# Optimization experiments

Measured on AMD Instinct MI355X. Metric: run time of the kernel, lower is better.

## Reference

```python
import jax, jax.numpy as jnp
import numpy as np

B, D, E, K = 8192, 1024, 8, 5  # batch, in_dim, num_size_classes, num_depth_classes
H = max(64, D)                 # hidden = max(64, in_dim)
EPS = 1e-8


def ordinal_logits_to_probs(logits, num_classes):
    # logits: [B, K-1] cumulative ordinal logits -> [B, K] class probs
    q = jax.nn.sigmoid(logits)
    probs = jnp.concatenate(
        [1.0 - q[:, :1], q[:, :-1] - q[:, 1:], q[:, -1:]], axis=1
    )  # [B, K]
    probs = jnp.clip(probs, EPS)
    return probs / jnp.clip(probs.sum(axis=1, keepdims=True), EPS)


def setup_inputs() -> dict:
    key = jax.random.key(0)
    kx, ks, k1, k2 = jax.random.split(key, 4)
    x = jax.random.normal(kx, (B, D), dtype=jnp.float32)
    size_idx = jax.random.randint(ks, (B,), 0, E, dtype=jnp.int64)
    # per-expert 2-layer MLP params: Linear(D,H) -> ReLU -> Linear(H,K-1)
    W1 = jax.random.normal(k1, (E, D, H), dtype=jnp.float32) / np.sqrt(D)
    b1 = jnp.zeros((E, H), dtype=jnp.float32)
    W2 = jax.random.normal(k2, (E, H, K - 1), dtype=jnp.float32) / np.sqrt(H)
    b2 = jnp.zeros((E, K - 1), dtype=jnp.float32)
    return {"x": x, "size_idx": size_idx, "W1": W1, "b1": b1, "W2": W2, "b2": b2}


def reference(x, size_idx, W1, b1, W2, b2):
    # Hard routing: each token gets the output of expert size_idx[b].
    # Dense all-expert compute + per-token select (same math as mask/gather/scatter,
    # dropout is inference-mode identity).
    h = jax.nn.relu(jnp.einsum('bd,edh->beh', x, W1) + b1)      # [B, E, H]
    all_logits = jnp.einsum('beh,ehk->bek', h, W2) + b2          # [B, E, K-1]
    idx = size_idx.astype(jnp.int32)[:, None, None]              # [B, 1, 1]
    logits = jnp.take_along_axis(all_logits, idx, axis=1)[:, 0]  # [B, K-1]
    probs = ordinal_logits_to_probs(logits, K)                   # [B, K]
    return logits, probs
```

## Files before the change

kernel.cpp:

```cpp
#include <hip/hip_runtime.h>
#include <cstdint>
#include <cstddef>

#define Bn 8192
#define Dn 1024
#define Hn 1024
#define En 8
#define MT 128
#define NB 16
#define MTILES (Bn / MT + En)
#define PERM_N (Bn + En * MT)

typedef unsigned short u16;
typedef __bf16 bf16x8 __attribute__((ext_vector_type(8)));
typedef float f32x4 __attribute__((ext_vector_type(4)));
typedef unsigned short ushort8 __attribute__((ext_vector_type(8)));

__device__ __forceinline__ u16 f2bf(float f) {
  unsigned int u = __float_as_uint(f);
  unsigned int r = u + 0x7fffu + ((u >> 16) & 1u);
  return (u16)(r >> 16);
}

__device__ __forceinline__ void gld16(const void* g, void* l) {
  __builtin_amdgcn_global_load_lds(
      (const __attribute__((address_space(1))) void*)g,
      (__attribute__((address_space(3))) void*)l, 16, 0, 0);
}

#define PIPE_BARRIER_VM4() do {                    \
    asm volatile("" ::: "memory");                 \
    __builtin_amdgcn_s_waitcnt(0x0F74);            \
    __builtin_amdgcn_s_barrier();                  \
    asm volatile("" ::: "memory");                 \
  } while (0)
#define PIPE_BARRIER_VM0() do {                    \
    asm volatile("" ::: "memory");                 \
    __builtin_amdgcn_s_waitcnt(0x0F70);            \
    __builtin_amdgcn_s_barrier();                  \
    asm volatile("" ::: "memory");                 \
  } while (0)

__global__ __launch_bounds__(1024) void route_k(const int* __restrict__ sidx,
                                                int* __restrict__ off,
                                                int* __restrict__ perm) {
  __shared__ int hist[16][En];
  __shared__ int base[16][En];
  __shared__ int eoff[En + 1];
  int t = threadIdx.x;
  int wv = t >> 6;
  if (t < 16 * En) ((int*)hist)[t] = 0;
#pragma unroll
  for (int i = 0; i < PERM_N / 1024; i++) perm[t + i * 1024] = -1;
  __syncthreads();
  int e8[8], r8[8];
#pragma unroll
  for (int i = 0; i < 8; i++) {
    int e = sidx[t + i * 1024];
    e8[i] = e;
    r8[i] = atomicAdd(&hist[wv][e], 1);
  }
  __syncthreads();
  if (t < En) {
    int s = 0;
    for (int w = 0; w < 16; w++) { base[w][t] = s; s += hist[w][t]; }
    hist[0][t] = s;
  }
  __syncthreads();
  if (t == 0) {
    int o = 0;
    for (int e = 0; e < En; e++) {
      eoff[e] = o; off[e] = o;
      o += (hist[0][e] + MT - 1) & ~(MT - 1);
    }
    eoff[En] = o; off[En] = o;
  }
  __syncthreads();
#pragma unroll
  for (int i = 0; i < 8; i++) {
    int e = e8[i];
    perm[eoff[e] + base[wv][e] + r8[i]] = t + i * 1024;
  }
}

__global__ __launch_bounds__(256) void cvt_xp_k(const float* __restrict__ x,
                                                const int* __restrict__ perm,
                                                u16* __restrict__ xbp) {
  size_t idx = ((size_t)blockIdx.x * 256 + threadIdx.x) * 8;
  int p = (int)(idx >> 10);
  int col = (int)(idx & 1023);
  int tok = perm[p];
  ushort8 o;
  if (tok < 0) {
    o = (ushort8){0, 0, 0, 0, 0, 0, 0, 0};
  } else {
    const float* src = x + ((size_t)tok << 10) + col;
    float4 a = *(const float4*)src;
    float4 b = *(const float4*)(src + 4);
    o[0] = f2bf(a.x); o[1] = f2bf(a.y); o[2] = f2bf(a.z); o[3] = f2bf(a.w);
    o[4] = f2bf(b.x); o[5] = f2bf(b.y); o[6] = f2bf(b.z); o[7] = f2bf(b.w);
  }
  *(ushort8*)(xbp + idx) = o;
}

__global__ __launch_bounds__(256) void cvt_w1_k(const float* __restrict__ W1,
                                                u16* __restrict__ W1t) {
  __shared__ float tile[64][65];
  int e = blockIdx.z;
  int k0 = blockIdx.y * 64;
  int n0 = blockIdx.x * 64;
  int c4 = (threadIdx.x & 15) * 4;
  int r0 = threadIdx.x >> 4;
  const float* src = W1 + ((size_t)e << 20) + (size_t)k0 * Hn + n0;
#pragma unroll
  for (int i = 0; i < 4; i++) {
    int r = r0 + i * 16;
    float4 v = *(const float4*)(src + (size_t)r * Hn + c4);
    tile[r][c4 + 0] = v.x; tile[r][c4 + 1] = v.y;
    tile[r][c4 + 2] = v.z; tile[r][c4 + 3] = v.w;
  }
  __syncthreads();
  u16* dst = W1t + ((size_t)e << 20) + (size_t)n0 * Dn + k0;
#pragma unroll
  for (int i = 0; i < 4; i++) {
    int h = r0 + i * 16;
    ushort4 o;
    o.x = f2bf(tile[c4 + 0][h]);
    o.y = f2bf(tile[c4 + 1][h]);
    o.z = f2bf(tile[c4 + 2][h]);
    o.w = f2bf(tile[c4 + 3][h]);
    *(ushort4*)(dst + (size_t)h * Dn + c4) = o;
  }
}

__global__ __launch_bounds__(256) void gemm_k(
    const u16* __restrict__ xbp, const u16* __restrict__ w1t,
    const float* __restrict__ b1, const float* __restrict__ w2,
    const int* __restrict__ off, float* __restrict__ partials) {
  __shared__ u16 As[3][4096];
  __shared__ u16 Bs[3][4096];

  int n0 = blockIdx.x * 128;
  int row0 = blockIdx.y * MT;
  if (row0 >= off[En]) return;
  int e = 0;
  while (row0 >= off[e + 1]) e++;

  int tid = threadIdx.x;
  int lane = tid & 63, w = tid >> 6;
  int wm = w >> 1, wn = w & 1;

  int srow = lane >> 2;
  int slot = lane & 3;
  int scol = (slot ^ ((srow >> 1) & 3)) * 8;
  const u16* aG[2]; const u16* bG[2];
  int lOff[2];
#pragma unroll
  for (int j = 0; j < 2; j++) {
    int rl = 32 * w + 16 * j + srow;
    aG[j] = xbp + (size_t)(row0 + rl) * Dn + scol;
    bG[j] = w1t + ((size_t)e << 20) + (size_t)(n0 + rl) * Dn + scol;
    lOff[j] = (32 * w + 16 * j) * 32;
  }

  f32x4 acc[4][4];
#pragma unroll
  for (int i = 0; i < 4; i++)
#pragma unroll
    for (int j = 0; j < 4; j++)
      acc[i][j] = (f32x4){0.f, 0.f, 0.f, 0.f};

  int fr = lane & 15;
  int qf = lane >> 4;
  int qs = (qf ^ ((fr >> 1) & 3)) * 8;
  int offA[4], offB[4];
#pragma unroll
  for (int i = 0; i < 4; i++)
    offA[i] = (wm * 64 + i * 16 + fr) * 32 + qs;
#pragma unroll
  for (int j = 0; j < 4; j++)
    offB[j] = (wn * 64 + j * 16 + fr) * 32 + qs;

#pragma unroll
  for (int it = 0; it < 2; it++) {
    int ko = it * 32;
    gld16(aG[0] + ko, (u16*)As[it] + lOff[0]);
    gld16(aG[1] + ko, (u16*)As[it] + lOff[1]);
    gld16(bG[0] + ko, (u16*)Bs[it] + lOff[0]);
    gld16(bG[1] + ko, (u16*)Bs[it] + lOff[1]);
  }

#pragma unroll
  for (int i = 0; i < 31; i++) {
    PIPE_BARRIER_VM4();
    if (i + 2 < 32) {
      int s = (i + 2) % 3;
      int ko = (i + 2) * 32;
      gld16(aG[0] + ko, (u16*)As[s] + lOff[0]);
      gld16(aG[1] + ko, (u16*)As[s] + lOff[1]);
      gld16(bG[0] + ko, (u16*)Bs[s] + lOff[0]);
      gld16(bG[1] + ko, (u16*)Bs[s] + lOff[1]);
    }
    const u16* Ab = (const u16*)As[i % 3];
    const u16* Bb = (const u16*)Bs[i % 3];
    bf16x8 af[4], bfr[4];
#pragma unroll
    for (int ii = 0; ii < 4; ii++) af[ii] = *(const bf16x8*)(Ab + offA[ii]);
#pragma unroll
    for (int jj = 0; jj < 4; jj++) bfr[jj] = *(const bf16x8*)(Bb + offB[jj]);
#pragma unroll
    for (int ii = 0; ii < 4; ii++)
#pragma unroll
      for (int jj = 0; jj < 4; jj++)
        acc[ii][jj] = __builtin_amdgcn_mfma_f32_16x16x32_bf16(af[ii], bfr[jj], acc[ii][jj], 0, 0, 0);
  }
  {
    PIPE_BARRIER_VM0();
    const u16* Ab = (const u16*)As[31 % 3];
    const u16* Bb = (const u16*)Bs[31 % 3];
    bf16x8 af[4], bfr[4];
#pragma unroll
    for (int ii = 0; ii < 4; ii++) af[ii] = *(const bf16x8*)(Ab + offA[ii]);
#pragma unroll
    for (int jj = 0; jj < 4; jj++) bfr[jj] = *(const bf16x8*)(Bb + offB[jj]);
#pragma unroll
    for (int ii = 0; ii < 4; ii++)
#pragma unroll
      for (int jj = 0; jj < 4; jj++)
        acc[ii][jj] = __builtin_amdgcn_mfma_f32_16x16x32_bf16(af[ii], bfr[jj], acc[ii][jj], 0, 0, 0);
  }

  int fq = lane >> 4;
  float4 w2v[4]; float b1v[4];
#pragma unroll
  for (int j = 0; j < 4; j++) {
    int col = n0 + wn * 64 + j * 16 + fr;
    w2v[j] = *(const float4*)(w2 + ((size_t)e * Hn + col) * 4);
    b1v[j] = b1[(size_t)e * Hn + col];
  }
  int chunk = blockIdx.x * 2 + wn;
#pragma unroll
  for (int i = 0; i < 4; i++) {
    int rbase = wm * 64 + i * 16 + fq * 4;
#pragma unroll
    for (int r = 0; r < 4; r++) {
      float s0 = 0.f, s1 = 0.f, s2 = 0.f, s3 = 0.f;
#pragma unroll
      for (int j = 0; j < 4; j++) {
        float h = acc[i][j][r] + b1v[j];
        h = fmaxf(h, 0.f);
        s0 = fmaf(h, w2v[j].x, s0);
        s1 = fmaf(h, w2v[j].y, s1);
        s2 = fmaf(h, w2v[j].z, s2);
        s3 = fmaf(h, w2v[j].w, s3);
      }
#pragma unroll
      for (int m = 1; m < 16; m <<= 1) {
        s0 += __shfl_xor(s0, m);
        s1 += __shfl_xor(s1, m);
        s2 += __shfl_xor(s2, m);
        s3 += __shfl_xor(s3, m);
      }
      if (fr == 0) {
        int row = row0 + rbase + r;
        *(float4*)(partials + ((size_t)row * NB + chunk) * 4) =
            make_float4(s0, s1, s2, s3);
      }
    }
  }
}

__global__ void probs_k(const float* __restrict__ partials,
                        const int* __restrict__ perm, const int* __restrict__ off,
                        const int* __restrict__ sidx, const float* __restrict__ b2,
                        float* __restrict__ out) {
  int p = blockIdx.x * blockDim.x + threadIdx.x;
  if (p >= off[En]) return;
  int tok = perm[p];
  if (tok < 0) return;
  int e = sidx[tok];
  float s0 = 0.f, s1 = 0.f, s2 = 0.f, s3 = 0.f;
#pragma unroll
  for (int nb = 0; nb < NB; nb++) {
    float4 v = *(const float4*)(partials + ((size_t)p * NB + nb) * 4);
    s0 += v.x; s1 += v.y; s2 += v.z; s3 += v.w;
  }
  float l0 = s0 + b2[e * 4 + 0];
  float l1 = s1 + b2[e * 4 + 1];
  float l2 = s2 + b2[e * 4 + 2];
  float l3 = s3 + b2[e * 4 + 3];
  out[tok * 4 + 0] = l0; out[tok * 4 + 1] = l1;
  out[tok * 4 + 2] = l2; out[tok * 4 + 3] = l3;
  float q0 = 1.f / (1.f + expf(-l0));
  float q1 = 1.f / (1.f + expf(-l1));
  float q2 = 1.f / (1.f + expf(-l2));
  float q3 = 1.f / (1.f + expf(-l3));
  const float eps = 1e-8f;
  float p0 = fmaxf(1.f - q0, eps);
  float p1 = fmaxf(q0 - q1, eps);
  float p2 = fmaxf(q1 - q2, eps);
  float p3 = fmaxf(q2 - q3, eps);
  float p4 = fmaxf(q3, eps);
  float s = p0 + p1 + p2 + p3 + p4;
  float inv = 1.f / fmaxf(s, eps);
  float* pr = out + (size_t)Bn * 4 + (size_t)tok * 5;
  pr[0] = p0 * inv; pr[1] = p1 * inv; pr[2] = p2 * inv;
  pr[3] = p3 * inv; pr[4] = p4 * inv;
}

extern "C" void kernel_launch(void* const* d_in, const int* in_sizes, int n_in,
                              void* d_out, int out_size, void* d_ws, size_t ws_size,
                              hipStream_t stream) {
  const float* x  = (const float*)d_in[0];
  const int* sidx = (const int*)d_in[1];
  const float* W1 = (const float*)d_in[2];
  const float* b1 = (const float*)d_in[3];
  const float* W2 = (const float*)d_in[4];
  const float* b2 = (const float*)d_in[5];
  float* out = (float*)d_out;

  uint8_t* w = (uint8_t*)d_ws;
  int* off  = (int*)(w + 64);
  int* perm = (int*)(w + 512);
  u16* xbp      = (u16*)(w + 40960);
  u16* w1t      = (u16*)(w + 18919424);
  float* parts  = (float*)(w + 35700736);

  route_k<<<1, 1024, 0, stream>>>(sidx, off, perm);
  cvt_xp_k<<<(PERM_N * Dn) / (256 * 8), 256, 0, stream>>>(x, perm, xbp);
  cvt_w1_k<<<dim3(Hn / 64, Dn / 64, En), 256, 0, stream>>>(W1, w1t);
  gemm_k<<<dim3(Hn / 128, MTILES), 256, 0, stream>>>(xbp, w1t, b1, W2, off, parts);
  probs_k<<<(PERM_N + 255) / 256, 256, 0, stream>>>(parts, perm, off, sidx, b2, out);
}
```

Before: 160.6 us.

## Parallelize routing, fuse W1 conversion with histogram, deepen GEMM pipeline to 4 stages

Replaces the single-block route kernel with a multi-block histogram, fused into the W1 transpose/convert kernel, followed by a multi-block ranking kernel that uses global atomics. The gather kernel now handles one row per block. The GEMM's LDS ring grows from 3 to 4 stages with a prefetch distance of 3, which adds shared memory and deeper in-flight loads. A memset and an extra launch are added, and token order within an expert becomes nondeterministic.

```diff
diff --git a/kernel.cpp b/kernel.cpp
--- a/kernel.cpp
+++ b/kernel.cpp
@@ -7,9 +7,9 @@
 #define Hn 1024
 #define En 8
 #define MT 128
+#define MTILES (PERM_N / MT)
+#define PERM_N (Bn + En * MT)
 #define NB 16
-#define MTILES (Bn / MT + En)
-#define PERM_N (Bn + En * MT)
 
 typedef unsigned short u16;
 typedef __bf16 bf16x8 __attribute__((ext_vector_type(8)));
@@ -28,108 +28,133 @@
       (__attribute__((address_space(3))) void*)l, 16, 0, 0);
 }
 
-#define PIPE_BARRIER_VM4() do {                    \
+#define PIPE_WAIT_BARRIER(imm) do {                \
     asm volatile("" ::: "memory");                 \
-    __builtin_amdgcn_s_waitcnt(0x0F74);            \
+    __builtin_amdgcn_s_waitcnt(imm);               \
     __builtin_amdgcn_s_barrier();                  \
     asm volatile("" ::: "memory");                 \
   } while (0)
-#define PIPE_BARRIER_VM0() do {                    \
-    asm volatile("" ::: "memory");                 \
-    __builtin_amdgcn_s_waitcnt(0x0F70);            \
-    __builtin_amdgcn_s_barrier();                  \
-    asm volatile("" ::: "memory");                 \
-  } while (0)
-
-__global__ __launch_bounds__(1024) void route_k(const int* __restrict__ sidx,
-                                                int* __restrict__ off,
-                                                int* __restrict__ perm) {
-  __shared__ int hist[16][En];
-  __shared__ int base[16][En];
-  __shared__ int eoff[En + 1];
+
+__global__ __launch_bounds__(256) void prep_k(const int* __restrict__ sidx,
+                                              const float* __restrict__ W1,
+                                              u16* __restrict__ w1t,
+                                              int* __restrict__ cnt) {
+  int bid = blockIdx.x;
   int t = threadIdx.x;
-  int wv = t >> 6;
-  if (t < 16 * En) ((int*)hist)[t] = 0;
-#pragma unroll
-  for (int i = 0; i < PERM_N / 1024; i++) perm[t + i * 1024] = -1;
-  __syncthreads();
-  int e8[8], r8[8];
-#pragma unroll
-  for (int i = 0; i < 8; i++) {
-    int e = sidx[t + i * 1024];
-    e8[i] = e;
-    r8[i] = atomicAdd(&hist[wv][e], 1);
-  }
-  __syncthreads();
-  if (t < En) {
-    int s = 0;
-    for (int w = 0; w < 16; w++) { base[w][t] = s; s += hist[w][t]; }
-    hist[0][t] = s;
-  }
-  __syncthreads();
-  if (t == 0) {
-    int o = 0;
-    for (int e = 0; e < En; e++) {
-      eoff[e] = o; off[e] = o;
-      o += (hist[0][e] + MT - 1) & ~(MT - 1);
-    }
-    eoff[En] = o; off[En] = o;
-  }
-  __syncthreads();
-#pragma unroll
-  for (int i = 0; i < 8; i++) {
-    int e = e8[i];
-    perm[eoff[e] + base[wv][e] + r8[i]] = t + i * 1024;
-  }
-}
-
-__global__ __launch_bounds__(256) void cvt_xp_k(const float* __restrict__ x,
+  if (bid < 8) {
+    __shared__ int hist[4][En];
+    int wv = t >> 6;
+    if (t < 4 * En) ((int*)hist)[t] = 0;
+    __syncthreads();
+#pragma unroll
+    for (int i = 0; i < 4; i++) {
+      int e = sidx[bid * 1024 + t + i * 256];
+      atomicAdd(&hist[wv][e], 1);
+    }
+    __syncthreads();
+    if (t < En) {
+      int s = hist[0][t] + hist[1][t] + hist[2][t] + hist[3][t];
+      atomicAdd(&cnt[t], s);
+    }
+  } else {
+    __shared__ float tile[64][65];
+    int wb = bid - 8;
+    int e = wb >> 8;
+    int k0 = ((wb >> 4) & 15) * 64;
+    int n0 = (wb & 15) * 64;
+    int c4 = (t & 15) * 4;
+    int r0 = t >> 4;
+    const float* src = W1 + ((size_t)e << 20) + (size_t)k0 * Hn + n0;
+#pragma unroll
+    for (int i = 0; i < 4; i++) {
+      int r = r0 + i * 16;
+      float4 v = *(const float4*)(src + (size_t)r * Hn + c4);
+      tile[r][c4 + 0] = v.x; tile[r][c4 + 1] = v.y;
+      tile[r][c4 + 2] = v.z; tile[r][c4 + 3] = v.w;
+    }
+    __syncthreads();
+    u16* dst = w1t + ((size_t)e << 20) + (size_t)n0 * Dn + k0;
+#pragma unroll
+    for (int i = 0; i < 4; i++) {
+      int h = r0 + i * 16;
+      ushort4 o;
+      o.x = f2bf(tile[c4 + 0][h]);
+      o.y = f2bf(tile[c4 + 1][h]);
+      o.z = f2bf(tile[c4 + 2][h]);
+      o.w = f2bf(tile[c4 + 3][h]);
+      *(ushort4*)(dst + (size_t)h * Dn + c4) = o;
+    }
+  }
+}
+
+__global__ __launch_bounds__(256) void rank_k(const int* __restrict__ sidx,
+                                              const int* __restrict__ cnt,
+                                              int* __restrict__ gcur,
+                                              int* __restrict__ off,
+                                              int* __restrict__ perm) {
+  int b = blockIdx.x, t = threadIdx.x;
+  int offl[En + 1];
+  int o = 0;
+#pragma unroll
+  for (int e = 0; e < En; e++) { offl[e] = o; o += (cnt[e] + MT - 1) & ~(MT - 1); }
+  offl[En] = o;
+
+  if (b < 32) {
+    __shared__ int hist[4][En];
+    __shared__ int wbase[4][En];
+    __shared__ int bbase[En];
+    int wv = t >> 6;
+    if (t < 4 * En) ((int*)hist)[t] = 0;
+    __syncthreads();
+    int tok = b * 256 + t;
+    int e = sidx[tok];
+    int r = atomicAdd(&hist[wv][e], 1);
+    __syncthreads();
+    if (t < En) {
+      int s = 0;
+#pragma unroll
+      for (int w = 0; w < 4; w++) { wbase[w][t] = s; s += hist[w][t]; }
+      bbase[t] = atomicAdd(&gcur[t], s);
+    }
+    __syncthreads();
+    int eo = offl[0];
+    int sel = e;
+    eo = (sel == 0) ? offl[0] : (sel == 1) ? offl[1] : (sel == 2) ? offl[2] :
+         (sel == 3) ? offl[3] : (sel == 4) ? offl[4] : (sel == 5) ? offl[5] :
+         (sel == 6) ? offl[6] : offl[7];
+    int dest = eo + bbase[e] + wbase[wv][e] + r;
+    perm[dest] = tok;
+  } else {
+    int e = b - 32;
+    int start = 0, end = 0, o2 = 0;
+#pragma unroll
+    for (int i = 0; i < En; i++) {
+      int pad = (cnt[i] + MT - 1) & ~(MT - 1);
+      if (i == e) { start = o2 + cnt[i]; end = o2 + pad; }
+      o2 += pad;
+    }
+    for (int p = start + t; p < end; p += 256) perm[p] = -1;
+    if (e == 0 && t == 0) {
+#pragma unroll
+      for (int i = 0; i <= En; i++) off[i] = offl[i];
+    }
+  }
+}
+
+__global__ __launch_bounds__(256) void gather_k(const float* __restrict__ x,
                                                 const int* __restrict__ perm,
                                                 u16* __restrict__ xbp) {
-  size_t idx = ((size_t)blockIdx.x * 256 + threadIdx.x) * 8;
-  int p = (int)(idx >> 10);
-  int col = (int)(idx & 1023);
+  int p = blockIdx.x;
+  int t = threadIdx.x;
   int tok = perm[p];
-  ushort8 o;
+  u16* dst = xbp + ((size_t)p << 10) + t * 4;
   if (tok < 0) {
-    o = (ushort8){0, 0, 0, 0, 0, 0, 0, 0};
+    *(ushort4*)dst = (ushort4){0, 0, 0, 0};
   } else {
-    const float* src = x + ((size_t)tok << 10) + col;
-    float4 a = *(const float4*)src;
-    float4 b = *(const float4*)(src + 4);
-    o[0] = f2bf(a.x); o[1] = f2bf(a.y); o[2] = f2bf(a.z); o[3] = f2bf(a.w);
-    o[4] = f2bf(b.x); o[5] = f2bf(b.y); o[6] = f2bf(b.z); o[7] = f2bf(b.w);
-  }
-  *(ushort8*)(xbp + idx) = o;
-}
-
-__global__ __launch_bounds__(256) void cvt_w1_k(const float* __restrict__ W1,
-                                                u16* __restrict__ W1t) {
-  __shared__ float tile[64][65];
-  int e = blockIdx.z;
-  int k0 = blockIdx.y * 64;
-  int n0 = blockIdx.x * 64;
-  int c4 = (threadIdx.x & 15) * 4;
-  int r0 = threadIdx.x >> 4;
-  const float* src = W1 + ((size_t)e << 20) + (size_t)k0 * Hn + n0;
-#pragma unroll
-  for (int i = 0; i < 4; i++) {
-    int r = r0 + i * 16;
-    float4 v = *(const float4*)(src + (size_t)r * Hn + c4);
-    tile[r][c4 + 0] = v.x; tile[r][c4 + 1] = v.y;
-    tile[r][c4 + 2] = v.z; tile[r][c4 + 3] = v.w;
-  }
-  __syncthreads();
-  u16* dst = W1t + ((size_t)e << 20) + (size_t)n0 * Dn + k0;
-#pragma unroll
-  for (int i = 0; i < 4; i++) {
-    int h = r0 + i * 16;
+    float4 v = *(const float4*)(x + ((size_t)tok << 10) + t * 4);
     ushort4 o;
-    o.x = f2bf(tile[c4 + 0][h]);
-    o.y = f2bf(tile[c4 + 1][h]);
-    o.z = f2bf(tile[c4 + 2][h]);
-    o.w = f2bf(tile[c4 + 3][h]);
-    *(ushort4*)(dst + (size_t)h * Dn + c4) = o;
+    o.x = f2bf(v.x); o.y = f2bf(v.y); o.z = f2bf(v.z); o.w = f2bf(v.w);
+    *(ushort4*)dst = o;
   }
 }
 
@@ -137,8 +162,8 @@
     const u16* __restrict__ xbp, const u16* __restrict__ w1t,
     const float* __restrict__ b1, const float* __restrict__ w2,
     const int* __restrict__ off, float* __restrict__ partials) {
-  __shared__ u16 As[3][4096];
-  __shared__ u16 Bs[3][4096];
+  __shared__ u16 As[4][4096];
+  __shared__ u16 Bs[4][4096];
 
   int n0 = blockIdx.x * 128;
   int row0 = blockIdx.y * MT;
@@ -182,7 +207,7 @@
     offB[j] = (wn * 64 + j * 16 + fr) * 32 + qs;
 
 #pragma unroll
-  for (int it = 0; it < 2; it++) {
+  for (int it = 0; it < 3; it++) {
     int ko = it * 32;
     gld16(aG[0] + ko, (u16*)As[it] + lOff[0]);
     gld16(aG[1] + ko, (u16*)As[it] + lOff[1]);
@@ -191,18 +216,20 @@
   }
 
 #pragma unroll
-  for (int i = 0; i < 31; i++) {
-    PIPE_BARRIER_VM4();
-    if (i + 2 < 32) {
-      int s = (i + 2) % 3;
-      int ko = (i + 2) * 32;
+  for (int i = 0; i < 32; i++) {
+    if (i <= 29)      PIPE_WAIT_BARRIER(0x0F78);
+    else if (i == 30) PIPE_WAIT_BARRIER(0x0F74);
+    else              PIPE_WAIT_BARRIER(0x0F70);
+    if (i + 3 < 32) {
+      int s = (i + 3) & 3;
+      int ko = (i + 3) * 32;
       gld16(aG[0] + ko, (u16*)As[s] + lOff[0]);
       gld16(aG[1] + ko, (u16*)As[s] + lOff[1]);
       gld16(bG[0] + ko, (u16*)Bs[s] + lOff[0]);
       gld16(bG[1] + ko, (u16*)Bs[s] + lOff[1]);
     }
-    const u16* Ab = (const u16*)As[i % 3];
-    const u16* Bb = (const u16*)Bs[i % 3];
+    const u16* Ab = (const u16*)As[i & 3];
+    const u16* Bb = (const u16*)Bs[i & 3];
     bf16x8 af[4], bfr[4];
 #pragma unroll
     for (int ii = 0; ii < 4; ii++) af[ii] = *(const bf16x8*)(Ab + offA[ii]);
@@ -214,23 +241,7 @@
       for (int jj = 0; jj < 4; jj++)
         acc[ii][jj] = __builtin_amdgcn_mfma_f32_16x16x32_bf16(af[ii], bfr[jj], acc[ii][jj], 0, 0, 0);
   }
-  {
-    PIPE_BARRIER_VM0();
-    const u16* Ab = (const u16*)As[31 % 3];
-    const u16* Bb = (const u16*)Bs[31 % 3];
-    bf16x8 af[4], bfr[4];
-#pragma unroll
-    for (int ii = 0; ii < 4; ii++) af[ii] = *(const bf16x8*)(Ab + offA[ii]);
-#pragma unroll
-    for (int jj = 0; jj < 4; jj++) bfr[jj] = *(const bf16x8*)(Bb + offB[jj]);
-#pragma unroll
-    for (int ii = 0; ii < 4; ii++)
-#pragma unroll
-      for (int jj = 0; jj < 4; jj++)
-        acc[ii][jj] = __builtin_amdgcn_mfma_f32_16x16x32_bf16(af[ii], bfr[jj], acc[ii][jj], 0, 0, 0);
-  }
-
-  int fq = lane >> 4;
+
   float4 w2v[4]; float b1v[4];
 #pragma unroll
   for (int j = 0; j < 4; j++) {
@@ -241,7 +252,7 @@
   int chunk = blockIdx.x * 2 + wn;
 #pragma unroll
   for (int i = 0; i < 4; i++) {
-    int rbase = wm * 64 + i * 16 + fq * 4;
+    int rbase = wm * 64 + i * 16 + qf * 4;
 #pragma unroll
     for (int r = 0; r < 4; r++) {
       float s0 = 0.f, s1 = 0.f, s2 = 0.f, s3 = 0.f;
@@ -320,15 +331,19 @@
   float* out = (float*)d_out;
 
   uint8_t* w = (uint8_t*)d_ws;
+  int* cnt  = (int*)(w + 0);
+  int* gcur = (int*)(w + 32);
   int* off  = (int*)(w + 64);
   int* perm = (int*)(w + 512);
-  u16* xbp      = (u16*)(w + 40960);
-  u16* w1t      = (u16*)(w + 18919424);
-  float* parts  = (float*)(w + 35700736);
-
-  route_k<<<1, 1024, 0, stream>>>(sidx, off, perm);
-  cvt_xp_k<<<(PERM_N * Dn) / (256 * 8), 256, 0, stream>>>(x, perm, xbp);
-  cvt_w1_k<<<dim3(Hn / 64, Dn / 64, En), 256, 0, stream>>>(W1, w1t);
+  u16* xbp     = (u16*)(w + 40960);
+  u16* w1t     = (u16*)(w + 18915328);
+  float* parts = (float*)(w + 35692544);
+
+  hipMemsetAsync(w, 0, 64, stream);
+
+  prep_k<<<8 + 2048, 256, 0, stream>>>(sidx, W1, w1t, cnt);
+  rank_k<<<40, 256, 0, stream>>>(sidx, cnt, gcur, off, perm);
+  gather_k<<<PERM_N, 256, 0, stream>>>(x, perm, xbp);
   gemm_k<<<dim3(Hn / 128, MTILES), 256, 0, stream>>>(xbp, w1t, b1, W2, off, parts);
   probs_k<<<(PERM_N + 255) / 256, 256, 0, stream>>>(parts, perm, off, sidx, b2, out);
 }
```

After: 171.6 us. +6.9%, slower.
